# Optimization experiments

Hardware: AMD Instinct MI355X
Metric: run time of the kernel (lower is better)

Reference implementation:

```python
import jax, jax.numpy as jnp
import numpy as np

H = 896          # hidden_size
S = H // 2       # split_size = 448
Q = 256          # quantisation
B = 16384        # batch (parallel sampling streams)


def setup_inputs() -> dict:
    key = jax.random.key(0)
    ks = jax.random.split(key, 16)
    sc = 0.02
    return {
        "prev_y": jax.random.uniform(ks[0], (B, 2), dtype=jnp.float32),
        "prev_hidden": jax.random.normal(ks[1], (B, H), dtype=jnp.float32),
        "current_coarse": jax.random.uniform(ks[2], (B, 1), dtype=jnp.float32),
        # torch Linear weights are [out_features, in_features]
        "R_w": sc * jax.random.normal(ks[3], (3 * H, H), dtype=jnp.float32),
        "Ic_w": sc * jax.random.normal(ks[4], (3 * S, 2), dtype=jnp.float32),
        "If_w": sc * jax.random.normal(ks[5], (3 * S, 3), dtype=jnp.float32),
        "bias_u": jnp.zeros((H,), jnp.float32),
        "bias_r": jnp.zeros((H,), jnp.float32),
        "bias_e": jnp.zeros((H,), jnp.float32),
        "O1_w": sc * jax.random.normal(ks[6], (S, S), dtype=jnp.float32),
        "O1_b": jnp.zeros((S,), jnp.float32),
        "O2_w": sc * jax.random.normal(ks[7], (Q, S), dtype=jnp.float32),
        "O2_b": jnp.zeros((Q,), jnp.float32),
        "O3_w": sc * jax.random.normal(ks[8], (S, S), dtype=jnp.float32),
        "O3_b": jnp.zeros((S,), jnp.float32),
        "O4_w": sc * jax.random.normal(ks[9], (Q, S), dtype=jnp.float32),
        "O4_b": jnp.zeros((Q,), jnp.float32),
    }


def reference(prev_y, prev_hidden, current_coarse,
              R_w, Ic_w, If_w, bias_u, bias_r, bias_e,
              O1_w, O1_b, O2_w, O2_b, O3_w, O3_b, O4_w, O4_b):
    # recurrent projection: [B,H] @ [H,3H] -> [B,3H]
    R_hidden = prev_hidden @ R_w.T
    R_u, R_r, R_e = jnp.split(R_hidden, 3, axis=1)

    # coarse input projection: [B,2] -> [B,3S]
    cproj = prev_y @ Ic_w.T
    Ic_u, Ic_r, Ic_e = jnp.split(cproj, 3, axis=1)

    # fine input projection: [B,3] -> [B,3S]
    fine_in = jnp.concatenate([prev_y, current_coarse], axis=1)
    fproj = fine_in @ If_w.T
    If_u, If_r, If_e = jnp.split(fproj, 3, axis=1)

    I_u = jnp.concatenate([Ic_u, If_u], axis=1)  # [B,H]
    I_r = jnp.concatenate([Ic_r, If_r], axis=1)
    I_e = jnp.concatenate([Ic_e, If_e], axis=1)

    u = jax.nn.sigmoid(R_u + I_u + bias_u)
    r = jax.nn.sigmoid(R_r + I_r + bias_r)
    e = jnp.tanh(r * R_e + I_e + bias_e)
    hidden = u * prev_hidden + (1.0 - u) * e  # [B,H]

    h_coarse, h_fine = jnp.split(hidden, 2, axis=1)  # [B,S] each
    out_coarse = jax.nn.relu(h_coarse @ O1_w.T + O1_b) @ O2_w.T + O2_b  # [B,Q]
    out_fine = jax.nn.relu(h_fine @ O3_w.T + O3_b) @ O4_w.T + O4_b      # [B,Q]
    return (out_coarse, out_fine, hidden)
```

## Files before the change

kernel.cpp:

```cpp
#include <hip/hip_runtime.h>
#include <hip/hip_bf16.h>
#include <cstdint>

#define BB 16384
#define HH 896
#define SS 448
#define QQ 256
#define NPAD 2816

typedef __attribute__((ext_vector_type(4))) float f32x4;
typedef __attribute__((ext_vector_type(8))) short bf16x8;

__device__ __forceinline__ short f2bf(float f){
  union { float f; uint32_t u; } x; x.f = f;
  uint32_t r = (x.u + 0x7fffu + ((x.u >> 16) & 1u)) >> 16;
  return (short)r;
}
__device__ __forceinline__ float bf2f(short b){
  union { uint32_t u; float f; } x; x.u = ((uint32_t)(uint16_t)b) << 16;
  return x.f;
}

__global__ __launch_bounds__(256)
void castall_kernel(const float* __restrict__ ph, short* __restrict__ Ah,
                    const float* __restrict__ Rw, short* __restrict__ Rwh,
                    const float* __restrict__ O1w, short* __restrict__ O1b,
                    const float* __restrict__ O3w, short* __restrict__ O3b,
                    const float* __restrict__ O2w, short* __restrict__ O2b,
                    const float* __restrict__ O4w, short* __restrict__ O4b)
{
  int u = blockIdx.x * 256 + threadIdx.x;
  auto cp4 = [](short* d, const float* s, int jd, int js){
    float4 v = reinterpret_cast<const float4*>(s)[js];
    short4 o; o.x = f2bf(v.x); o.y = f2bf(v.y); o.z = f2bf(v.z); o.w = f2bf(v.w);
    reinterpret_cast<short4*>(d)[jd] = o;
  };
  auto z4 = [](short* d, int jd){
    short4 o; o.x = 0; o.y = 0; o.z = 0; o.w = 0;
    reinterpret_cast<short4*>(d)[jd] = o;
  };
  if (u < 3670016) { cp4(Ah, ph, u, u); return; }
  u -= 3670016;
  if (u < 602112) { cp4(Rwh, Rw, u, u); return; }
  u -= 602112;
  if (u < 28672) { z4(Rwh, 602112 + u); return; }
  u -= 28672;
  if (u < 57344) { if (u < 50176) cp4(O1b, O1w, u, u); else z4(O1b, u); return; }
  u -= 57344;
  if (u < 57344) { if (u < 50176) cp4(O3b, O3w, u, u); else z4(O3b, u); return; }
  u -= 57344;
  if (u < 32768) {
    int r = u >> 7, c4 = u & 127;
    if (c4 < 112) cp4(O2b, O2w, u, r * 112 + c4); else z4(O2b, u);
    return;
  }
  u -= 32768;
  if (u < 32768) {
    int r = u >> 7, c4 = u & 127;
    if (c4 < 112) cp4(O4b, O4w, u, r * 112 + c4); else z4(O4b, u);
    return;
  }
}

template<int EP>
__global__ __launch_bounds__(512, 2)
void gemm256_bt(const short* __restrict__ A0p, const short* __restrict__ A1p, int lda,
                const short* __restrict__ B0p, const short* __restrict__ B1p, int ldb,
                void* __restrict__ C0p, void* __restrict__ C1p, int ldc,
                const float* __restrict__ bias0, const float* __restrict__ bias1, int nbias,
                int Nvalid, int K, int nbn)
{
  const int zi = (EP == 2) ? (blockIdx.z & 1) : blockIdx.z;
  const int zh = (EP == 2) ? (blockIdx.z >> 1) : 0;
  const short* A  = zi ? A1p : A0p;
  const short* Bt = zi ? B1p : B0p;
  void* Cv        = zi ? C1p : C0p;
  const float* bias = zi ? bias1 : bias0;

  __shared__ short smem[65536];
  const int tid = threadIdx.x;
  const int w  = tid >> 6, ln = tid & 63;
  const int wr = w >> 2,  wc = w & 3;
  const int lr = ln & 15;
  const int lg = ln >> 4;
  const int srow = ln >> 3;
  const int sgc  = (ln & 7) ^ srow;

  int wg = blockIdx.x;
  const int cpx = gridDim.x >> 3;
  wg = (wg & 7) * cpx + (wg >> 3);
  const int bm = wg / nbn, bn = wg - bm * nbn;
  const long m0 = (long)bm * 256 + (long)zh * 8192;
  const long n0 = (long)bn * 256;

  f32x4 acc[8][4] = {};

  auto stage = [&](const short* __restrict__ src, int ld, long rbase, int k0,
                   int lbase , int h) {
#pragma unroll
    for (int i = 0; i < 2; ++i) {
      const int rloc = h * 128 + i * 64 + w * 8;
      const short* g = src + (rbase + rloc + srow) * (long)ld + k0 + sgc * 8;
      __builtin_amdgcn_global_load_lds(
          (const __attribute__((address_space(1))) void*)g,
          (__attribute__((address_space(3))) void*)&smem[lbase + rloc * 64],
          16, 0, 0);
    }
  };
  auto rd = [&](int lbase, int r, int ks) -> bf16x8 {
    const int gc = ks * 4 + lg;
    return *reinterpret_cast<const bf16x8*>(&smem[lbase + r * 64 + ((gc ^ (r & 7)) << 3)]);
  };

  const int NT = K >> 6;
  stage(A,  lda, m0, 0, 0,     0);
  stage(Bt, ldb, n0, 0, 32768, 0);
  stage(Bt, ldb, n0, 0, 32768, 1);
  stage(A,  lda, m0, 0, 0,     1);
  asm volatile("s_waitcnt vmcnt(2)" ::: "memory");
  __builtin_amdgcn_s_barrier();
  asm volatile("" ::: "memory");

  for (int j = 0; j < NT; ++j) {
    const int Ab = (j & 1) * 16384;
    const int Bb = 32768 + (j & 1) * 16384;
    const int An = ((j + 1) & 1) * 16384;
    const int Bn = 32768 + ((j + 1) & 1) * 16384;
    const bool pf = (j + 1 < NT);
    const int k1 = (j + 1) << 6;
    bf16x8 b[4][2];

    __builtin_amdgcn_s_setprio(1);
    {
#pragma unroll
      for (int n = 0; n < 4; ++n)
#pragma unroll
        for (int ks = 0; ks < 2; ++ks)
          b[n][ks] = rd(Bb, wc * 64 + n * 16 + lr, ks);
      if (pf) {
        stage(A,  lda, m0, k1, An, 0);
        stage(Bt, ldb, n0, k1, Bn, 0);
        stage(Bt, ldb, n0, k1, Bn, 1);
        stage(A,  lda, m0, k1, An, 1);
      }
#pragma unroll
      for (int q = 0; q < 2; ++q) {
        bf16x8 a[2][2];
#pragma unroll
        for (int dm = 0; dm < 2; ++dm)
#pragma unroll
          for (int ks = 0; ks < 2; ++ks)
            a[dm][ks] = rd(Ab, q * 64 + dm * 32 + wr * 16 + lr, ks);
#pragma unroll
        for (int dm = 0; dm < 2; ++dm)
#pragma unroll
          for (int n = 0; n < 4; ++n)
#pragma unroll
            for (int ks = 0; ks < 2; ++ks)
              acc[2 * q + dm][n] = __builtin_amdgcn_mfma_f32_16x16x32_bf16(
                  a[dm][ks], b[n][ks], acc[2 * q + dm][n], 0, 0, 0);
      }
    }
    __builtin_amdgcn_s_setprio(0);
    if (pf) asm volatile("s_waitcnt vmcnt(8)" ::: "memory");
    else    asm volatile("s_waitcnt vmcnt(0)" ::: "memory");
    __builtin_amdgcn_s_barrier();
    asm volatile("" ::: "memory");

    __builtin_amdgcn_s_setprio(1);
    {
#pragma unroll
      for (int q = 2; q < 4; ++q) {
        bf16x8 a[2][2];
#pragma unroll
        for (int dm = 0; dm < 2; ++dm)
#pragma unroll
          for (int ks = 0; ks < 2; ++ks)
            a[dm][ks] = rd(Ab, q * 64 + dm * 32 + wr * 16 + lr, ks);
#pragma unroll
        for (int dm = 0; dm < 2; ++dm)
#pragma unroll
          for (int n = 0; n < 4; ++n)
#pragma unroll
            for (int ks = 0; ks < 2; ++ks)
              acc[2 * q + dm][n] = __builtin_amdgcn_mfma_f32_16x16x32_bf16(
                  a[dm][ks], b[n][ks], acc[2 * q + dm][n], 0, 0, 0);
      }
    }
    __builtin_amdgcn_s_setprio(0);
    asm volatile("s_waitcnt vmcnt(2)" ::: "memory");
    __builtin_amdgcn_s_barrier();
    asm volatile("" ::: "memory");
  }

  if (EP == 2) {
    const int lc = ln & 15, rg = lg * 4;
#pragma unroll
    for (int n = 0; n < 4; ++n) {
      const long col = n0 + wc * 64 + n * 16 + lc;
      const float bv = bias[col];
#pragma unroll
      for (int m = 0; m < 8; ++m) {
        const long row = m0 + m * 32 + wr * 16 + rg;
#pragma unroll
        for (int reg = 0; reg < 4; ++reg)
          ((float*)Cv)[(row + reg) * (long)ldc + col] = acc[m][n][reg] + bv;
      }
    }
    return;
  }

#pragma unroll
  for (int n = 0; n < 4; ++n) {
    const int col = wc * 64 + n * 16 + lr;
    const int gc = col >> 3, c7 = col & 7;
    float bv = 0.f;
    if (EP == 1) {
      const long gcol = n0 + col;
      bv = (gcol < nbias) ? bias[gcol] : 0.f;
    }
#pragma unroll
    for (int m = 0; m < 8; ++m) {
      const int row = m * 32 + wr * 16 + lg * 4;
#pragma unroll
      for (int reg = 0; reg < 4; ++reg) {
        float v = acc[m][n][reg];
        if (EP == 1) { v += bv; v = v > 0.f ? v : 0.f; }
        const int rr = row + reg;
        smem[rr * 256 + ((gc ^ ((rr >> 1) & 7)) << 3) + c7] = f2bf(v);
      }
    }
  }
  __builtin_amdgcn_s_barrier();
  const int rt = tid >> 5;
  const int ctg = (tid & 31);
  const long colg = n0 + ctg * 8;
  if (colg < Nvalid) {
#pragma unroll
    for (int p = 0; p < 16; ++p) {
      const int row = p * 16 + rt;
      bf16x8 v = *reinterpret_cast<const bf16x8*>(
          &smem[row * 256 + ((ctg ^ ((row >> 1) & 7)) << 3)]);
      *reinterpret_cast<bf16x8*>(&((short*)Cv)[(m0 + row) * (long)ldc + colg]) = v;
    }
  }
}

__global__ __launch_bounds__(256)
void gates_kernel(const float* __restrict__ prev_y,
                  const short* __restrict__ Ah,
                  const float* __restrict__ ccoarse,
                  const float* __restrict__ Icw,
                  const float* __restrict__ Ifw,
                  const float* __restrict__ bu,
                  const float* __restrict__ br,
                  const float* __restrict__ be,
                  const short* __restrict__ Rh,
                  float* __restrict__ hid_out,
                  short* __restrict__ hid_bf)
{
  const int v = blockIdx.x * 256 + threadIdx.x;
  const int b = v / 112;
  const int h0 = (v - b * 112) * 8;
  const long rbase = (long)b * (3 * HH);

  const bf16x8 ru8 = *reinterpret_cast<const bf16x8*>(Rh + rbase + h0);
  const bf16x8 rr8 = *reinterpret_cast<const bf16x8*>(Rh + rbase + HH + h0);
  const bf16x8 re8 = *reinterpret_cast<const bf16x8*>(Rh + rbase + 2 * HH + h0);
  const bf16x8 ah8 = *reinterpret_cast<const bf16x8*>(Ah + (long)b * HH + h0);
  const float py0 = prev_y[2 * b], py1 = prev_y[2 * b + 1], c0 = ccoarse[b];

  float iu[8], ir[8], ie[8];
  if (h0 < SS) {
    const float4* cu = reinterpret_cast<const float4*>(Icw + 2 * h0);
    const float4* cr = reinterpret_cast<const float4*>(Icw + 2 * (SS + h0));
    const float4* ce = reinterpret_cast<const float4*>(Icw + 2 * (2 * SS + h0));
#pragma unroll
    for (int q = 0; q < 4; ++q) {
      float4 a = cu[q]; iu[2*q] = py0*a.x + py1*a.y; iu[2*q+1] = py0*a.z + py1*a.w;
      float4 r = cr[q]; ir[2*q] = py0*r.x + py1*r.y; ir[2*q+1] = py0*r.z + py1*r.w;
      float4 e = ce[q]; ie[2*q] = py0*e.x + py1*e.y; ie[2*q+1] = py0*e.z + py1*e.w;
    }
  } else {
    const int j0 = h0 - SS;
    const float* fu = Ifw + 3 * j0;
    const float* fr = Ifw + 3 * (SS + j0);
    const float* fe = Ifw + 3 * (2 * SS + j0);
#pragma unroll
    for (int j = 0; j < 8; ++j) {
      iu[j] = py0 * fu[3*j] + py1 * fu[3*j+1] + c0 * fu[3*j+2];
      ir[j] = py0 * fr[3*j] + py1 * fr[3*j+1] + c0 * fr[3*j+2];
      ie[j] = py0 * fe[3*j] + py1 * fe[3*j+1] + c0 * fe[3*j+2];
    }
  }
  const float4* bu4 = reinterpret_cast<const float4*>(bu + h0);
  const float4* br4 = reinterpret_cast<const float4*>(br + h0);
  const float4* be4 = reinterpret_cast<const float4*>(be + h0);
  float buv[8], brv[8], bev[8];
  { float4 a = bu4[0], b2 = bu4[1];
    buv[0]=a.x; buv[1]=a.y; buv[2]=a.z; buv[3]=a.w; buv[4]=b2.x; buv[5]=b2.y; buv[6]=b2.z; buv[7]=b2.w; }
  { float4 a = br4[0], b2 = br4[1];
    brv[0]=a.x; brv[1]=a.y; brv[2]=a.z; brv[3]=a.w; brv[4]=b2.x; brv[5]=b2.y; brv[6]=b2.z; brv[7]=b2.w; }
  { float4 a = be4[0], b2 = be4[1];
    bev[0]=a.x; bev[1]=a.y; bev[2]=a.z; bev[3]=a.w; bev[4]=b2.x; bev[5]=b2.y; bev[6]=b2.z; bev[7]=b2.w; }

  float hd[8];
  bf16x8 hb;
#pragma unroll
  for (int j = 0; j < 8; ++j) {
    float u = 1.f / (1.f + __expf(-(bf2f(ru8[j]) + iu[j] + buv[j])));
    float r = 1.f / (1.f + __expf(-(bf2f(rr8[j]) + ir[j] + brv[j])));
    float e = tanhf(r * bf2f(re8[j]) + ie[j] + bev[j]);
    hd[j] = u * bf2f(ah8[j]) + (1.f - u) * e;
    hb[j] = f2bf(hd[j]);
  }
  float4* ho = reinterpret_cast<float4*>(hid_out + (long)b * HH + h0);
  ho[0] = make_float4(hd[0], hd[1], hd[2], hd[3]);
  ho[1] = make_float4(hd[4], hd[5], hd[6], hd[7]);
  *reinterpret_cast<bf16x8*>(hid_bf + (long)b * HH + h0) = hb;
}

extern "C" void kernel_launch(void* const* d_in, const int* in_sizes, int n_in,
                              void* d_out, int out_size, void* d_ws, size_t ws_size,
                              hipStream_t stream)
{
  (void)in_sizes; (void)n_in; (void)out_size; (void)ws_size;
  const float* prev_y      = (const float*)d_in[0];
  const float* prev_hidden = (const float*)d_in[1];
  const float* ccoarse     = (const float*)d_in[2];
  const float* R_w  = (const float*)d_in[3];
  const float* Ic_w = (const float*)d_in[4];
  const float* If_w = (const float*)d_in[5];
  const float* bu   = (const float*)d_in[6];
  const float* br   = (const float*)d_in[7];
  const float* be   = (const float*)d_in[8];
  const float* O1w  = (const float*)d_in[9];
  const float* O1b  = (const float*)d_in[10];
  const float* O2w  = (const float*)d_in[11];
  const float* O2b  = (const float*)d_in[12];
  const float* O3w  = (const float*)d_in[13];
  const float* O3b  = (const float*)d_in[14];
  const float* O4w  = (const float*)d_in[15];
  const float* O4b  = (const float*)d_in[16];

  float* out_coarse = (float*)d_out;
  float* out_fine   = out_coarse + (long)BB * QQ;
  float* hidden     = out_fine + (long)BB * QQ;

  char* ws = (char*)d_ws;
  short* Ah   = (short*)(ws + 0);
  short* Rwh  = (short*)(ws + 29360128);
  short* Rh   = (short*)(ws + 34406400);
  short* hidb = (short*)(ws + 122486784);
  short* O1wb = (short*)(ws + 151846912);
  short* O3wb = (short*)(ws + 152305664);
  short* O2wb = (short*)(ws + 152764416);
  short* O4wb = (short*)(ws + 153026560);
  short* t1   = (short*)(ws + 0);
  short* t2   = (short*)(ws + 16777216);

  castall_kernel<<<17504, 256, 0, stream>>>(prev_hidden, Ah, R_w, Rwh,
                                            O1w, O1wb, O3w, O3wb, O2w, O2wb, O4w, O4wb);

  gemm256_bt<0><<<dim3(704, 1, 1), 512, 0, stream>>>(
      Ah, Ah, HH, Rwh, Rwh, HH, Rh, Rh, 3 * HH,
      nullptr, nullptr, 0, 3 * HH, HH, 11);

  gates_kernel<<<BB * 112 / 256, 256, 0, stream>>>(prev_y, Ah, ccoarse,
                                                   Ic_w, If_w, bu, br, be, Rh, hidden, hidb);

  gemm256_bt<1><<<dim3(128, 1, 2), 512, 0, stream>>>(
      hidb, hidb + 448, HH, O1wb, O3wb, 448, t1, t2, 512,
      O1b, O3b, 448, 512, 448, 2);

  gemm256_bt<2><<<dim3(32, 1, 4), 512, 0, stream>>>(
      t1, t2, 512, O2wb, O4wb, 512, out_coarse, out_fine, QQ,
      O2b, O4b, QQ, QQ, 512, 1);
}
```

Measured before the change: 216.4 us.

## Load B fragments directly to registers and triple-buffer A tiles in LDS

The GEMM main loop stops staging the B (weight) tile through LDS. Each wave now loads its B fragments straight from global memory into registers, double-buffered across iterations, while A tiles go through a three-stage LDS ring with prefetch two steps ahead and one barrier per K-step. LDS use drops from 128KB to 96KB, so the epilogue writes output in two row halves to fit in the smaller buffer. The aim is fewer barriers and less LDS traffic, which could help occupancy. The cost is more register pressure and uncoalesced global reads of B that rely on the cache.

Result: slower. 268.0 us (+23.8%).

```diff
diff --git a/kernel.cpp b/kernel.cpp
--- a/kernel.cpp
+++ b/kernel.cpp
@@ -77,7 +77,7 @@
   void* Cv        = zi ? C1p : C0p;
   const float* bias = zi ? bias1 : bias0;
 
-  __shared__ short smem[65536];
+  __shared__ short smem[49152];
   const int tid = threadIdx.x;
   const int w  = tid >> 6, ln = tid & 63;
   const int wr = w >> 2,  wc = w & 3;
@@ -94,104 +94,78 @@
   const long n0 = (long)bn * 256;
 
   f32x4 acc[8][4] = {};
-
-  auto stage = [&](const short* __restrict__ src, int ld, long rbase, int k0,
-                   int lbase , int h) {
-#pragma unroll
-    for (int i = 0; i < 2; ++i) {
-      const int rloc = h * 128 + i * 64 + w * 8;
-      const short* g = src + (rbase + rloc + srow) * (long)ld + k0 + sgc * 8;
+  bf16x8 bA[4][2], bB[4][2];
+
+  auto stageA = [&](int k0, int base ) {
+#pragma unroll
+    for (int i = 0; i < 4; ++i) {
+      const int rloc = i * 64 + w * 8;
+      const short* g = A + (m0 + rloc + srow) * (long)lda + k0 + sgc * 8;
       __builtin_amdgcn_global_load_lds(
           (const __attribute__((address_space(1))) void*)g,
-          (__attribute__((address_space(3))) void*)&smem[lbase + rloc * 64],
+          (__attribute__((address_space(3))) void*)&smem[base + rloc * 64],
           16, 0, 0);
     }
   };
-  auto rd = [&](int lbase, int r, int ks) -> bf16x8 {
+  auto loadB = [&](int k0, bf16x8 (&dst)[4][2]) {
+#pragma unroll
+    for (int n = 0; n < 4; ++n)
+#pragma unroll
+      for (int ks = 0; ks < 2; ++ks)
+        dst[n][ks] = *reinterpret_cast<const bf16x8*>(
+            &Bt[(n0 + wc * 64 + n * 16 + lr) * (long)ldb + k0 + ks * 32 + lg * 8]);
+  };
+  auto rd = [&](int base, int r, int ks) -> bf16x8 {
     const int gc = ks * 4 + lg;
-    return *reinterpret_cast<const bf16x8*>(&smem[lbase + r * 64 + ((gc ^ (r & 7)) << 3)]);
+    return *reinterpret_cast<const bf16x8*>(&smem[base + r * 64 + ((gc ^ (r & 7)) << 3)]);
   };
 
   const int NT = K >> 6;
-  stage(A,  lda, m0, 0, 0,     0);
-  stage(Bt, ldb, n0, 0, 32768, 0);
-  stage(Bt, ldb, n0, 0, 32768, 1);
-  stage(A,  lda, m0, 0, 0,     1);
-  asm volatile("s_waitcnt vmcnt(2)" ::: "memory");
+
+  auto body = [&](int j, bf16x8 (&bcur)[4][2], bf16x8 (&bnxt)[4][2]) {
+    const bool pf1 = (j + 1 < NT), pf2 = (j + 2 < NT);
+    if (pf1) loadB((j + 1) << 6, bnxt);
+    __builtin_amdgcn_sched_barrier(0);
+    if (pf2) stageA((j + 2) << 6, ((j + 2) % 3) * 16384);
+    __builtin_amdgcn_sched_barrier(0);
+    const int cb = (j % 3) * 16384;
+    __builtin_amdgcn_s_setprio(1);
+#pragma unroll
+    for (int q = 0; q < 4; ++q) {
+      bf16x8 a[2][2];
+#pragma unroll
+      for (int dm = 0; dm < 2; ++dm)
+#pragma unroll
+        for (int ks = 0; ks < 2; ++ks)
+          a[dm][ks] = rd(cb, q * 64 + dm * 32 + wr * 16 + lr, ks);
+#pragma unroll
+      for (int dm = 0; dm < 2; ++dm)
+#pragma unroll
+        for (int n = 0; n < 4; ++n)
+#pragma unroll
+          for (int ks = 0; ks < 2; ++ks)
+            acc[2 * q + dm][n] = __builtin_amdgcn_mfma_f32_16x16x32_bf16(
+                a[dm][ks], bcur[n][ks], acc[2 * q + dm][n], 0, 0, 0);
+    }
+    __builtin_amdgcn_s_setprio(0);
+    __builtin_amdgcn_sched_barrier(0);
+    if (pf2) asm volatile("s_waitcnt vmcnt(4)" ::: "memory");
+    else     asm volatile("s_waitcnt vmcnt(0)" ::: "memory");
+    __builtin_amdgcn_s_barrier();
+    asm volatile("" ::: "memory");
+  };
+
+  loadB(0, bA);
+  __builtin_amdgcn_sched_barrier(0);
+  stageA(0, 0);
+  stageA(64, 16384);
+  asm volatile("s_waitcnt vmcnt(4)" ::: "memory");
   __builtin_amdgcn_s_barrier();
   asm volatile("" ::: "memory");
 
-  for (int j = 0; j < NT; ++j) {
-    const int Ab = (j & 1) * 16384;
-    const int Bb = 32768 + (j & 1) * 16384;
-    const int An = ((j + 1) & 1) * 16384;
-    const int Bn = 32768 + ((j + 1) & 1) * 16384;
-    const bool pf = (j + 1 < NT);
-    const int k1 = (j + 1) << 6;
-    bf16x8 b[4][2];
-
-    __builtin_amdgcn_s_setprio(1);
-    {
-#pragma unroll
-      for (int n = 0; n < 4; ++n)
-#pragma unroll
-        for (int ks = 0; ks < 2; ++ks)
-          b[n][ks] = rd(Bb, wc * 64 + n * 16 + lr, ks);
-      if (pf) {
-        stage(A,  lda, m0, k1, An, 0);
-        stage(Bt, ldb, n0, k1, Bn, 0);
-        stage(Bt, ldb, n0, k1, Bn, 1);
-        stage(A,  lda, m0, k1, An, 1);
-      }
-#pragma unroll
-      for (int q = 0; q < 2; ++q) {
-        bf16x8 a[2][2];
-#pragma unroll
-        for (int dm = 0; dm < 2; ++dm)
-#pragma unroll
-          for (int ks = 0; ks < 2; ++ks)
-            a[dm][ks] = rd(Ab, q * 64 + dm * 32 + wr * 16 + lr, ks);
-#pragma unroll
-        for (int dm = 0; dm < 2; ++dm)
-#pragma unroll
-          for (int n = 0; n < 4; ++n)
-#pragma unroll
-            for (int ks = 0; ks < 2; ++ks)
-              acc[2 * q + dm][n] = __builtin_amdgcn_mfma_f32_16x16x32_bf16(
-                  a[dm][ks], b[n][ks], acc[2 * q + dm][n], 0, 0, 0);
-      }
-    }
-    __builtin_amdgcn_s_setprio(0);
-    if (pf) asm volatile("s_waitcnt vmcnt(8)" ::: "memory");
-    else    asm volatile("s_waitcnt vmcnt(0)" ::: "memory");
-    __builtin_amdgcn_s_barrier();
-    asm volatile("" ::: "memory");
-
-    __builtin_amdgcn_s_setprio(1);
-    {
-#pragma unroll
-      for (int q = 2; q < 4; ++q) {
-        bf16x8 a[2][2];
-#pragma unroll
-        for (int dm = 0; dm < 2; ++dm)
-#pragma unroll
-          for (int ks = 0; ks < 2; ++ks)
-            a[dm][ks] = rd(Ab, q * 64 + dm * 32 + wr * 16 + lr, ks);
-#pragma unroll
-        for (int dm = 0; dm < 2; ++dm)
-#pragma unroll
-          for (int n = 0; n < 4; ++n)
-#pragma unroll
-            for (int ks = 0; ks < 2; ++ks)
-              acc[2 * q + dm][n] = __builtin_amdgcn_mfma_f32_16x16x32_bf16(
-                  a[dm][ks], b[n][ks], acc[2 * q + dm][n], 0, 0, 0);
-      }
-    }
-    __builtin_amdgcn_s_setprio(0);
-    asm volatile("s_waitcnt vmcnt(2)" ::: "memory");
-    __builtin_amdgcn_s_barrier();
-    asm volatile("" ::: "memory");
-  }
+  int j = 0;
+  for (; j + 1 < NT; j += 2) { body(j, bA, bB); body(j + 1, bB, bA); }
+  if (j < NT) body(j, bA, bB);
 
   if (EP == 2) {
     const int lc = ln & 15, rg = lg * 4;
@@ -211,38 +185,46 @@
   }
 
 #pragma unroll
-  for (int n = 0; n < 4; ++n) {
-    const int col = wc * 64 + n * 16 + lr;
-    const int gc = col >> 3, c7 = col & 7;
-    float bv = 0.f;
-    if (EP == 1) {
-      const long gcol = n0 + col;
-      bv = (gcol < nbias) ? bias[gcol] : 0.f;
-    }
-#pragma unroll
-    for (int m = 0; m < 8; ++m) {
-      const int row = m * 32 + wr * 16 + lg * 4;
-#pragma unroll
-      for (int reg = 0; reg < 4; ++reg) {
-        float v = acc[m][n][reg];
-        if (EP == 1) { v += bv; v = v > 0.f ? v : 0.f; }
-        const int rr = row + reg;
-        smem[rr * 256 + ((gc ^ ((rr >> 1) & 7)) << 3) + c7] = f2bf(v);
+  for (int h = 0; h < 2; ++h) {
+    if (wr == h) {
+#pragma unroll
+      for (int n = 0; n < 4; ++n) {
+        const int col = wc * 64 + n * 16 + lr;
+        const int gc = col >> 3, c7 = col & 7;
+        float bv = 0.f;
+        if (EP == 1) {
+          const long gcol = n0 + col;
+          bv = (gcol < nbias) ? bias[gcol] : 0.f;
+        }
+#pragma unroll
+        for (int m = 0; m < 8; ++m) {
+#pragma unroll
+          for (int reg = 0; reg < 4; ++reg) {
+            float v = acc[m][n][reg];
+            if (EP == 1) { v += bv; v = v > 0.f ? v : 0.f; }
+            const int rl = m * 16 + lg * 4 + reg;
+            smem[rl * 256 + ((gc ^ ((rl >> 1) & 7)) << 3) + c7] = f2bf(v);
+          }
+        }
       }
     }
-  }
-  __builtin_amdgcn_s_barrier();
-  const int rt = tid >> 5;
-  const int ctg = (tid & 31);
-  const long colg = n0 + ctg * 8;
-  if (colg < Nvalid) {
-#pragma unroll
-    for (int p = 0; p < 16; ++p) {
-      const int row = p * 16 + rt;
-      bf16x8 v = *reinterpret_cast<const bf16x8*>(
-          &smem[row * 256 + ((ctg ^ ((row >> 1) & 7)) << 3)]);
-      *reinterpret_cast<bf16x8*>(&((short*)Cv)[(m0 + row) * (long)ldc + colg]) = v;
-    }
+    __builtin_amdgcn_s_barrier();
+    asm volatile("" ::: "memory");
+    const int rt = tid >> 5;
+    const int ctg = tid & 31;
+    const long colg = n0 + ctg * 8;
+    if (colg < Nvalid) {
+#pragma unroll
+      for (int p = 0; p < 8; ++p) {
+        const int rl = p * 16 + rt;
+        bf16x8 v = *reinterpret_cast<const bf16x8*>(
+            &smem[rl * 256 + ((ctg ^ ((rl >> 1) & 7)) << 3)]);
+        const long grow = m0 + p * 32 + h * 16 + rt;
+        *reinterpret_cast<bf16x8*>(&((short*)Cv)[grow * (long)ldc + colg]) = v;
+      }
+    }
+    __builtin_amdgcn_s_barrier();
+    asm volatile("" ::: "memory");
   }
 }
 
```
